# Kernel tuning notes

Measured on AMD Instinct MI355X. Metric: run time of the kernel, lower is better.

Reference implementation:

```python
import jax, jax.numpy as jnp
import numpy as np

T, V, K = 128, 5023, 16  # time frames, FLAME vertices, max neighbors


def setup_inputs() -> dict:
    key = jax.random.key(0)
    k1, k2, k3, k4 = jax.random.split(key, 4)
    canonical = jax.random.normal(k1, (T, V, 3), dtype=jnp.float32)
    deformed = canonical + 0.1 * jax.random.normal(k2, (T, V, 3), dtype=jnp.float32)
    neighbors = jax.random.randint(k3, (V, K), 0, V)
    neighbors_mask = jax.random.bernoulli(k4, 0.8, (V, K))
    return {
        "canonical_vertices": canonical,
        "deformed_vertices": deformed,
        "neighbors": neighbors,
        "neighbors_mask": neighbors_mask,
    }


def _matrix_to_quaternion(M):
    """Rotation matrix [..., 3, 3] -> quaternion [..., 4] (w, x, y, z).
    Standard numerically-robust 4-candidate selection (pytorch3d style)."""
    m00, m01, m02 = M[..., 0, 0], M[..., 0, 1], M[..., 0, 2]
    m10, m11, m12 = M[..., 1, 0], M[..., 1, 1], M[..., 1, 2]
    m20, m21, m22 = M[..., 2, 0], M[..., 2, 1], M[..., 2, 2]
    q_abs = jnp.sqrt(jnp.clip(jnp.stack([
        1.0 + m00 + m11 + m22,
        1.0 + m00 - m11 - m22,
        1.0 - m00 + m11 - m22,
        1.0 - m00 - m11 + m22,
    ], axis=-1), 0.0, None))
    quat_by_rijk = jnp.stack([
        jnp.stack([q_abs[..., 0] ** 2, m21 - m12, m02 - m20, m10 - m01], -1),
        jnp.stack([m21 - m12, q_abs[..., 1] ** 2, m01 + m10, m02 + m20], -1),
        jnp.stack([m02 - m20, m10 + m01, q_abs[..., 2] ** 2, m12 + m21], -1),
        jnp.stack([m10 - m01, m20 + m02, m21 + m12, q_abs[..., 3] ** 2], -1),
    ], axis=-2)  # [..., 4, 4]
    floor = jnp.asarray(0.1, M.dtype)
    quat_candidates = quat_by_rijk / (2.0 * jnp.maximum(q_abs[..., None], floor))
    one_hot = jax.nn.one_hot(jnp.argmax(q_abs, axis=-1), 4, dtype=M.dtype)
    return jnp.sum(quat_candidates * one_hot[..., None], axis=-2)


def reference(canonical_vertices, deformed_vertices, neighbors, neighbors_mask):
    dtype = canonical_vertices.dtype
    maskf = neighbors_mask[..., None].astype(dtype)  # [V, K, 1]
    # gather neighbor positions, zeroing padded slots (matches torch code)
    p = canonical_vertices[:, neighbors, :] * maskf  # [T, V, K, 3]
    q = deformed_vertices[:, neighbors, :] * maskf   # [T, V, K, 3]
    # center on the vertex itself
    p_c = p - canonical_vertices[:, :, None, :]
    q_c = q - deformed_vertices[:, :, None, :]
    # per-vertex 3x3 covariance: p_centered^T @ q_centered
    cov = jnp.einsum('tvki,tvkj->tvij', p_c, q_c)  # [T, V, 3, 3]
    u, s, vh = jnp.linalg.svd(cov)
    det = jnp.linalg.det(u @ vh)  # det(u @ v^T), since v^T == vh
    ones = jnp.ones_like(det)
    d3 = jnp.where(jnp.abs(det - 1.0) > 1e-6, det, ones)
    # v @ diag(1, 1, d3) scales the columns of v
    col_scale = jnp.stack([ones, ones, d3], axis=-1)[..., None, :]  # [T,V,1,3]
    v = jnp.swapaxes(vh, -1, -2)
    rotation_matrix = (v * col_scale) @ jnp.swapaxes(u, -1, -2)  # [T,V,3,3]
    rotation = _matrix_to_quaternion(rotation_matrix)  # [T, V, 4]
    translation = deformed_vertices - canonical_vertices  # [T, V, 3]
    return rotation, translation
```

## Files before the change

### kernel.cpp

```cpp
#include <hip/hip_runtime.h>


namespace {
constexpr int T_FRAMES = 128;
constexpr int V_NUM    = 5023;
constexpr int K_NB     = 16;
constexpr int SLAB     = V_NUM * 3;
constexpr int SLAB_PAD = 15072;
constexpr int LDS_BYTES = (SLAB_PAD + SLAB) * 4;
}

__global__ __launch_bounds__(1024)
void mask_detect_kernel(const uint4* __restrict__ m, int* __restrict__ flag) {
    __shared__ int c_bool, c_f32;
    if (threadIdx.x == 0) { c_bool = 0; c_f32 = 0; }
    __syncthreads();
    int cb = 0, cf = 0;
    for (int i = threadIdx.x; i < V_NUM; i += 1024) {
        const uint4 w = m[i];
        const unsigned x0 = w.x, x1 = w.y, x2 = w.z, x3 = w.w;
        cb += (((x0 >> 8) & 0xffu) == 1u) + (((x0 >> 24) & 0xffu) == 1u);
        cb += (((x1 >> 8) & 0xffu) == 1u) + (((x1 >> 24) & 0xffu) == 1u);
        cb += (((x2 >> 8) & 0xffu) == 1u) + (((x2 >> 24) & 0xffu) == 1u);
        cb += (((x3 >> 8) & 0xffu) == 1u) + (((x3 >> 24) & 0xffu) == 1u);
        cf += ((x0 >> 24) == 0x3fu) + ((x1 >> 24) == 0x3fu);
        cf += ((x2 >> 24) == 0x3fu) + ((x3 >> 24) == 0x3fu);
    }
    atomicAdd(&c_bool, cb);
    atomicAdd(&c_f32, cf);
    __syncthreads();
    if (threadIdx.x == 0) {
        constexpr int nbytes = V_NUM * K_NB;
        int f = 0;
        if (c_bool > nbytes / 8)      f = 1;
        else if (c_f32 > nbytes / 16) f = 2;
        *flag = f;
    }
}

__global__ __launch_bounds__(1024)
void se3_extract_kernel(const float* __restrict__ cano,
                        const float* __restrict__ defo,
                        const int*   __restrict__ nbr,
                        const unsigned char* __restrict__ mask_raw,
                        const int*   __restrict__ mflag_p,
                        float* __restrict__ out) {
    extern __shared__ float lds[];
    float* __restrict__ lds_c = lds;
    float* __restrict__ lds_d = lds + SLAB_PAD;

    const int bid  = blockIdx.x;
    const int t    = bid & 127;
    const int half = bid >> 7;
    const int tid  = threadIdx.x;
    const int mflag = *mflag_p;

    const float* __restrict__ cfp = cano + (size_t)t * SLAB;
    const float* __restrict__ dfp = defo + (size_t)t * SLAB;
    for (int i = tid; i < SLAB; i += 1024) {
        lds_c[i] = cfp[i];
        lds_d[i] = dfp[i];
    }
    __syncthreads();

    const int vbeg = half ? 2512 : 0;
    const int vend = half ? V_NUM : 2512;

    for (int v = vbeg + tid; v < vend; v += 1024) {
        const float cvx = lds_c[v*3+0], cvy = lds_c[v*3+1], cvz = lds_c[v*3+2];
        const float dvx = lds_d[v*3+0], dvy = lds_d[v*3+1], dvz = lds_d[v*3+2];

        int nb[K_NB];
        {
            const int4* p4 = reinterpret_cast<const int4*>(nbr + (size_t)v * K_NB);
            #pragma unroll
            for (int j = 0; j < K_NB / 4; ++j) {
                const int4 q = p4[j];
                nb[j*4+0] = q.x; nb[j*4+1] = q.y; nb[j*4+2] = q.z; nb[j*4+3] = q.w;
            }
        }

        float mk[K_NB];
        if (mflag == 1) {
            const uint4 mw = *reinterpret_cast<const uint4*>(mask_raw + (size_t)v * K_NB);
            const unsigned w[4] = {mw.x, mw.y, mw.z, mw.w};
            #pragma unroll
            for (int j = 0; j < 4; ++j) {
                mk[j*4+0] = ((w[j]        & 0xffu) != 0u) ? 1.0f : 0.0f;
                mk[j*4+1] = (((w[j] >> 8 ) & 0xffu) != 0u) ? 1.0f : 0.0f;
                mk[j*4+2] = (((w[j] >> 16) & 0xffu) != 0u) ? 1.0f : 0.0f;
                mk[j*4+3] = (((w[j] >> 24) & 0xffu) != 0u) ? 1.0f : 0.0f;
            }
        } else if (mflag == 0) {
            const int* mp = reinterpret_cast<const int*>(mask_raw) + (size_t)v * K_NB;
            #pragma unroll
            for (int k = 0; k < K_NB; ++k) mk[k] = mp[k] ? 1.0f : 0.0f;
        } else {
            const float* mp = reinterpret_cast<const float*>(mask_raw) + (size_t)v * K_NB;
            #pragma unroll
            for (int k = 0; k < K_NB; ++k) mk[k] = (mp[k] != 0.0f) ? 1.0f : 0.0f;
        }

        float a00=0.f,a01=0.f,a02=0.f,a10=0.f,a11=0.f,a12=0.f,a20=0.f,a21=0.f,a22=0.f;
        #pragma unroll
        for (int k = 0; k < K_NB; ++k) {
            const int n3 = nb[k] * 3;
            const float m = mk[k];
            const float px = fmaf(lds_c[n3+0], m, -cvx);
            const float py = fmaf(lds_c[n3+1], m, -cvy);
            const float pz = fmaf(lds_c[n3+2], m, -cvz);
            const float qx = fmaf(lds_d[n3+0], m, -dvx);
            const float qy = fmaf(lds_d[n3+1], m, -dvy);
            const float qz = fmaf(lds_d[n3+2], m, -dvz);
            a00 = fmaf(px,qx,a00); a01 = fmaf(px,qy,a01); a02 = fmaf(px,qz,a02);
            a10 = fmaf(py,qx,a10); a11 = fmaf(py,qy,a11); a12 = fmaf(py,qz,a12);
            a20 = fmaf(pz,qx,a20); a21 = fmaf(pz,qy,a21); a22 = fmaf(pz,qz,a22);
        }

        float x00=a00, x01=a10, x02=a20;
        float x10=a01, x11=a11, x12=a21;
        float x20=a02, x21=a12, x22=a22;
        #pragma unroll
        for (int it = 0; it < 8; ++it) {
            const float c00 = x11*x22 - x12*x21;
            const float c01 = x12*x20 - x10*x22;
            const float c02 = x10*x21 - x11*x20;
            const float c10 = x02*x21 - x01*x22;
            const float c11 = x00*x22 - x02*x20;
            const float c12 = x01*x20 - x00*x21;
            const float c20 = x01*x12 - x02*x11;
            const float c21 = x02*x10 - x00*x12;
            const float c22 = x00*x11 - x01*x10;
            const float det = x00*c00 + x01*c01 + x02*c02;
            const float ad  = fmaxf(fabsf(det), 1e-30f);
            const float sd  = (det < 0.0f) ? -ad : ad;
            const float mu  = __builtin_amdgcn_exp2f(-0.3333333333f *
                                                     __builtin_amdgcn_logf(ad));
            const float hm  = 0.5f * mu;
            const float r   = 0.5f * __builtin_amdgcn_rcpf(mu * sd);
            x00 = hm*x00 + r*c00; x01 = hm*x01 + r*c01; x02 = hm*x02 + r*c02;
            x10 = hm*x10 + r*c10; x11 = hm*x11 + r*c11; x12 = hm*x12 + r*c12;
            x20 = hm*x20 + r*c20; x21 = hm*x21 + r*c21; x22 = hm*x22 + r*c22;
        }

        const float qa0 = sqrtf(fmaxf(1.0f + x00 + x11 + x22, 0.0f));
        const float qa1 = sqrtf(fmaxf(1.0f + x00 - x11 - x22, 0.0f));
        const float qa2 = sqrtf(fmaxf(1.0f - x00 + x11 - x22, 0.0f));
        const float qa3 = sqrtf(fmaxf(1.0f - x00 - x11 + x22, 0.0f));

        int best = 0; float bq = qa0;
        if (qa1 > bq) { best = 1; bq = qa1; }
        if (qa2 > bq) { best = 2; bq = qa2; }
        if (qa3 > bq) { best = 3; bq = qa3; }

        float r0, r1, r2, r3;
        if      (best == 0) { r0 = qa0*qa0; r1 = x21-x12; r2 = x02-x20; r3 = x10-x01; }
        else if (best == 1) { r0 = x21-x12; r1 = qa1*qa1; r2 = x01+x10; r3 = x02+x20; }
        else if (best == 2) { r0 = x02-x20; r1 = x10+x01; r2 = qa2*qa2; r3 = x12+x21; }
        else                { r0 = x10-x01; r1 = x20+x02; r2 = x21+x12; r3 = qa3*qa3; }
        const float qi = __builtin_amdgcn_rcpf(2.0f * fmaxf(bq, 0.1f));

        const size_t base_q = ((size_t)t * V_NUM + v) * 4;
        float4 qout;
        qout.x = r0 * qi; qout.y = r1 * qi; qout.z = r2 * qi; qout.w = r3 * qi;
        *reinterpret_cast<float4*>(out + base_q) = qout;

        const size_t base_t = (size_t)T_FRAMES * V_NUM * 4 + ((size_t)t * V_NUM + v) * 3;
        out[base_t+0] = dvx - cvx;
        out[base_t+1] = dvy - cvy;
        out[base_t+2] = dvz - cvz;
    }
}

extern "C" void kernel_launch(void* const* d_in, const int* in_sizes, int n_in,
                              void* d_out, int out_size, void* d_ws, size_t ws_size,
                              hipStream_t stream) {
    const float* cano = (const float*)d_in[0];
    const float* defo = (const float*)d_in[1];
    const int*   nbr  = (const int*)d_in[2];
    const unsigned char* mask = (const unsigned char*)d_in[3];
    float* out = (float*)d_out;
    int* flag = (int*)d_ws;

    static bool attr_set = false;
    if (!attr_set) {
        (void)hipFuncSetAttribute((const void*)se3_extract_kernel,
                                  hipFuncAttributeMaxDynamicSharedMemorySize,
                                  LDS_BYTES);
        attr_set = true;
    }

    mask_detect_kernel<<<1, 1024, 0, stream>>>((const uint4*)mask, flag);

    se3_extract_kernel<<<256, 1024, LDS_BYTES, stream>>>(cano, defo, nbr, mask,
                                                         flag, out);
}
```

Measured before the change: 106.4 us.

## Inline mask detection, pad LDS to float4, simplify polar Newton iteration

```diff
diff --git a/kernel.cpp b/kernel.cpp
--- a/kernel.cpp
+++ b/kernel.cpp
@@ -6,36 +6,7 @@
 constexpr int V_NUM    = 5023;
 constexpr int K_NB     = 16;
 constexpr int SLAB     = V_NUM * 3;
-constexpr int SLAB_PAD = 15072;
-constexpr int LDS_BYTES = (SLAB_PAD + SLAB) * 4;
-}
-
-__global__ __launch_bounds__(1024)
-void mask_detect_kernel(const uint4* __restrict__ m, int* __restrict__ flag) {
-    __shared__ int c_bool, c_f32;
-    if (threadIdx.x == 0) { c_bool = 0; c_f32 = 0; }
-    __syncthreads();
-    int cb = 0, cf = 0;
-    for (int i = threadIdx.x; i < V_NUM; i += 1024) {
-        const uint4 w = m[i];
-        const unsigned x0 = w.x, x1 = w.y, x2 = w.z, x3 = w.w;
-        cb += (((x0 >> 8) & 0xffu) == 1u) + (((x0 >> 24) & 0xffu) == 1u);
-        cb += (((x1 >> 8) & 0xffu) == 1u) + (((x1 >> 24) & 0xffu) == 1u);
-        cb += (((x2 >> 8) & 0xffu) == 1u) + (((x2 >> 24) & 0xffu) == 1u);
-        cb += (((x3 >> 8) & 0xffu) == 1u) + (((x3 >> 24) & 0xffu) == 1u);
-        cf += ((x0 >> 24) == 0x3fu) + ((x1 >> 24) == 0x3fu);
-        cf += ((x2 >> 24) == 0x3fu) + ((x3 >> 24) == 0x3fu);
-    }
-    atomicAdd(&c_bool, cb);
-    atomicAdd(&c_f32, cf);
-    __syncthreads();
-    if (threadIdx.x == 0) {
-        constexpr int nbytes = V_NUM * K_NB;
-        int f = 0;
-        if (c_bool > nbytes / 8)      f = 1;
-        else if (c_f32 > nbytes / 16) f = 2;
-        *flag = f;
-    }
+constexpr int LDS_BYTES = V_NUM * 16 * 2;
 }
 
 __global__ __launch_bounds__(1024)
@@ -43,23 +14,35 @@
                         const float* __restrict__ defo,
                         const int*   __restrict__ nbr,
                         const unsigned char* __restrict__ mask_raw,
-                        const int*   __restrict__ mflag_p,
                         float* __restrict__ out) {
-    extern __shared__ float lds[];
-    float* __restrict__ lds_c = lds;
-    float* __restrict__ lds_d = lds + SLAB_PAD;
+    extern __shared__ float4 lds4[];
+    float4* __restrict__ ldsc = lds4;
+    float4* __restrict__ ldsd = lds4 + V_NUM;
 
     const int bid  = blockIdx.x;
     const int t    = bid & 127;
     const int half = bid >> 7;
     const int tid  = threadIdx.x;
-    const int mflag = *mflag_p;
+
+    int mflag;
+    {
+        const unsigned w = reinterpret_cast<const unsigned*>(mask_raw)[tid & 63];
+        const bool isb = ((((w >> 8) & 0xffu) == 1u) | (((w >> 24) & 0xffu) == 1u));
+        const bool isf = ((w >> 24) == 0x3fu);
+        const unsigned long long mb = __ballot(isb);
+        const unsigned long long mf = __ballot(isf);
+        mflag = 0;
+        if (__popcll(mb) > 16)      mflag = 1;
+        else if (__popcll(mf) > 16) mflag = 2;
+    }
 
     const float* __restrict__ cfp = cano + (size_t)t * SLAB;
     const float* __restrict__ dfp = defo + (size_t)t * SLAB;
-    for (int i = tid; i < SLAB; i += 1024) {
-        lds_c[i] = cfp[i];
-        lds_d[i] = dfp[i];
+    for (int i = tid; i < V_NUM; i += 1024) {
+        const float* cp = cfp + i * 3;
+        ldsc[i] = make_float4(cp[0], cp[1], cp[2], 0.0f);
+        const float* dp = dfp + i * 3;
+        ldsd[i] = make_float4(dp[0], dp[1], dp[2], 0.0f);
     }
     __syncthreads();
 
@@ -67,8 +50,8 @@
     const int vend = half ? V_NUM : 2512;
 
     for (int v = vbeg + tid; v < vend; v += 1024) {
-        const float cvx = lds_c[v*3+0], cvy = lds_c[v*3+1], cvz = lds_c[v*3+2];
-        const float dvx = lds_d[v*3+0], dvy = lds_d[v*3+1], dvz = lds_d[v*3+2];
+        const float4 cv = ldsc[v];
+        const float4 dv = ldsd[v];
 
         int nb[K_NB];
         {
@@ -86,7 +69,7 @@
             const unsigned w[4] = {mw.x, mw.y, mw.z, mw.w};
             #pragma unroll
             for (int j = 0; j < 4; ++j) {
-                mk[j*4+0] = ((w[j]        & 0xffu) != 0u) ? 1.0f : 0.0f;
+                mk[j*4+0] = ((w[j]         & 0xffu) != 0u) ? 1.0f : 0.0f;
                 mk[j*4+1] = (((w[j] >> 8 ) & 0xffu) != 0u) ? 1.0f : 0.0f;
                 mk[j*4+2] = (((w[j] >> 16) & 0xffu) != 0u) ? 1.0f : 0.0f;
                 mk[j*4+3] = (((w[j] >> 24) & 0xffu) != 0u) ? 1.0f : 0.0f;
@@ -104,14 +87,16 @@
         float a00=0.f,a01=0.f,a02=0.f,a10=0.f,a11=0.f,a12=0.f,a20=0.f,a21=0.f,a22=0.f;
         #pragma unroll
         for (int k = 0; k < K_NB; ++k) {
-            const int n3 = nb[k] * 3;
+            const int n = nb[k];
             const float m = mk[k];
-            const float px = fmaf(lds_c[n3+0], m, -cvx);
-            const float py = fmaf(lds_c[n3+1], m, -cvy);
-            const float pz = fmaf(lds_c[n3+2], m, -cvz);
-            const float qx = fmaf(lds_d[n3+0], m, -dvx);
-            const float qy = fmaf(lds_d[n3+1], m, -dvy);
-            const float qz = fmaf(lds_d[n3+2], m, -dvz);
+            const float4 cp = ldsc[n];
+            const float4 dp = ldsd[n];
+            const float px = fmaf(cp.x, m, -cv.x);
+            const float py = fmaf(cp.y, m, -cv.y);
+            const float pz = fmaf(cp.z, m, -cv.z);
+            const float qx = fmaf(dp.x, m, -dv.x);
+            const float qy = fmaf(dp.y, m, -dv.y);
+            const float qz = fmaf(dp.z, m, -dv.z);
             a00 = fmaf(px,qx,a00); a01 = fmaf(px,qy,a01); a02 = fmaf(px,qz,a02);
             a10 = fmaf(py,qx,a10); a11 = fmaf(py,qy,a11); a12 = fmaf(py,qz,a12);
             a20 = fmaf(pz,qx,a20); a21 = fmaf(pz,qy,a21); a22 = fmaf(pz,qz,a22);
@@ -120,6 +105,18 @@
         float x00=a00, x01=a10, x02=a20;
         float x10=a01, x11=a11, x12=a21;
         float x20=a02, x21=a12, x22=a22;
+        {
+            const float d0 = x00*(x11*x22 - x12*x21)
+                           - x01*(x10*x22 - x12*x20)
+                           + x02*(x10*x21 - x11*x20);
+            const float ad = fmaxf(fabsf(d0), 1e-30f);
+            float mu = __builtin_amdgcn_exp2f(-0.3333333333f *
+                                              __builtin_amdgcn_logf(ad));
+            if (d0 < 0.0f) mu = -mu;
+            x00*=mu; x01*=mu; x02*=mu;
+            x10*=mu; x11*=mu; x12*=mu;
+            x20*=mu; x21*=mu; x22*=mu;
+        }
         #pragma unroll
         for (int it = 0; it < 8; ++it) {
             const float c00 = x11*x22 - x12*x21;
@@ -132,15 +129,10 @@
             const float c21 = x02*x10 - x00*x12;
             const float c22 = x00*x11 - x01*x10;
             const float det = x00*c00 + x01*c01 + x02*c02;
-            const float ad  = fmaxf(fabsf(det), 1e-30f);
-            const float sd  = (det < 0.0f) ? -ad : ad;
-            const float mu  = __builtin_amdgcn_exp2f(-0.3333333333f *
-                                                     __builtin_amdgcn_logf(ad));
-            const float hm  = 0.5f * mu;
-            const float r   = 0.5f * __builtin_amdgcn_rcpf(mu * sd);
-            x00 = hm*x00 + r*c00; x01 = hm*x01 + r*c01; x02 = hm*x02 + r*c02;
-            x10 = hm*x10 + r*c10; x11 = hm*x11 + r*c11; x12 = hm*x12 + r*c12;
-            x20 = hm*x20 + r*c20; x21 = hm*x21 + r*c21; x22 = hm*x22 + r*c22;
+            const float r   = 0.5f * __builtin_amdgcn_rcpf(det);
+            x00 = fmaf(0.5f, x00, r*c00); x01 = fmaf(0.5f, x01, r*c01); x02 = fmaf(0.5f, x02, r*c02);
+            x10 = fmaf(0.5f, x10, r*c10); x11 = fmaf(0.5f, x11, r*c11); x12 = fmaf(0.5f, x12, r*c12);
+            x20 = fmaf(0.5f, x20, r*c20); x21 = fmaf(0.5f, x21, r*c21); x22 = fmaf(0.5f, x22, r*c22);
         }
 
         const float qa0 = sqrtf(fmaxf(1.0f + x00 + x11 + x22, 0.0f));
@@ -166,9 +158,9 @@
         *reinterpret_cast<float4*>(out + base_q) = qout;
 
         const size_t base_t = (size_t)T_FRAMES * V_NUM * 4 + ((size_t)t * V_NUM + v) * 3;
-        out[base_t+0] = dvx - cvx;
-        out[base_t+1] = dvy - cvy;
-        out[base_t+2] = dvz - cvz;
+        out[base_t+0] = dv.x - cv.x;
+        out[base_t+1] = dv.y - cv.y;
+        out[base_t+2] = dv.z - cv.z;
     }
 }
 
@@ -180,7 +172,6 @@
     const int*   nbr  = (const int*)d_in[2];
     const unsigned char* mask = (const unsigned char*)d_in[3];
     float* out = (float*)d_out;
-    int* flag = (int*)d_ws;
 
     static bool attr_set = false;
     if (!attr_set) {
@@ -190,8 +181,5 @@
         attr_set = true;
     }
 
-    mask_detect_kernel<<<1, 1024, 0, stream>>>((const uint4*)mask, flag);
-
-    se3_extract_kernel<<<256, 1024, LDS_BYTES, stream>>>(cano, defo, nbr, mask,
-                                                         flag, out);
+    se3_extract_kernel<<<256, 1024, LDS_BYTES, stream>>>(cano, defo, nbr, mask, out);
 }
```

Result: faster. 91.63 us (-13.9%).
